# Performance work log

Measured on AMD Instinct MI355X. Metric: run time of the kernel, lower is better.

The kernel has to match this reference:

```python
import jax, jax.numpy as jnp
import numpy as np

B, T, D, K = 16, 2048, 256, 1024


def setup_inputs() -> dict:
    key = jax.random.key(0)
    k1, k2 = jax.random.split(key)
    z_e_x = jax.random.normal(k1, (B, T, D), dtype=jnp.float32)
    # torch init is uniform(-1/K, 1/K); use normal scaled similarly for a realistic trained codebook
    embedding = jax.random.normal(k2, (K, D), dtype=jnp.float32)
    return {"z_e_x": z_e_x, "embedding": embedding}


def _vq_indices(inputs_flat, codebook):
    codebook_sqr = jnp.sum(codebook * codebook, axis=1)            # [K]
    inputs_sqr = jnp.sum(inputs_flat * inputs_flat, axis=1, keepdims=True)  # [N,1]
    distances = inputs_sqr + codebook_sqr[None, :] - 2.0 * (inputs_flat @ codebook.T)  # [N,K]
    return jnp.argmin(distances, axis=1)                           # [N] int


def reference(z_e_x, embedding):
    Dd = embedding.shape[1]
    inputs_flat = z_e_x.reshape(-1, Dd)                 # [N, D]
    indices_flat = _vq_indices(inputs_flat, embedding)  # [N]
    codes = embedding[indices_flat].reshape(z_e_x.shape)  # gather lookup
    z_q_x = codes                                       # straight-through quantized output
    z_q_x_bar = codes                                   # eval mode: embedding unchanged, same gather
    indices = indices_flat.reshape(z_e_x.shape[:-1])
    return (z_q_x, z_q_x_bar, indices)
```

## Files before the change

### kernel.cpp

```cpp
#include <hip/hip_runtime.h>
#include <float.h>

constexpr int kD = 256;
constexpr int kK = 1024;
constexpr int kN = 16 * 2048;

using bf16x8 = __attribute__((ext_vector_type(8))) short;
using f32x16 = __attribute__((ext_vector_type(16))) float;
using u16x8  = __attribute__((ext_vector_type(8))) unsigned short;

__device__ __forceinline__ unsigned short f2bf(float x) {
    union { float f; unsigned u; } a; a.f = x;
    const unsigned u = a.u;
    return (unsigned short)((u + 0x7fffu + ((u >> 16) & 1u)) >> 16);
}
__device__ __forceinline__ float bf2f(unsigned short b) {
    union { unsigned u; float f; } a; a.u = ((unsigned)b) << 16;
    return a.f;
}

#define GLOAD_LDS16(GP, LP) \
    __builtin_amdgcn_global_load_lds((const __attribute__((address_space(1))) unsigned int*)(GP), \
                                     (__attribute__((address_space(3))) unsigned int*)(LP), 16, 0, 0)

__global__ void vq_split_kernel(const float* __restrict__ src,
                                unsigned short* __restrict__ oh,
                                unsigned short* __restrict__ om,
                                unsigned short* __restrict__ ol) {
    const int RB = blockIdx.x;
    const int t  = threadIdx.x;
    #pragma unroll
    for (int it = 0; it < 8; ++it) {
        const int u   = it * 256 + t;
        const int l   = u & 63;
        const int f   = (u >> 6) & 1;
        const int t16 = u >> 7;
        const int row = RB * 64 + f * 32 + (l & 31);
        const int d0  = t16 * 16 + (l >> 5) * 8;
        const float4 v0 = *reinterpret_cast<const float4*>(src + (size_t)row * kD + d0);
        const float4 v1 = *reinterpret_cast<const float4*>(src + (size_t)row * kD + d0 + 4);
        const float x[8] = {v0.x, v0.y, v0.z, v0.w, v1.x, v1.y, v1.z, v1.w};
        u16x8 H, M, L;
        #pragma unroll
        for (int e = 0; e < 8; ++e) {
            const unsigned short h = f2bf(x[e]);
            const float r1 = x[e] - bf2f(h);
            const unsigned short m = f2bf(r1);
            const float r2 = r1 - bf2f(m);
            const unsigned short lo = f2bf(r2);
            H[e] = (short)h; M[e] = (short)m; L[e] = (short)lo;
        }
        const size_t o = (size_t)RB * 16384 + (size_t)u * 8;
        *reinterpret_cast<u16x8*>(oh + o) = H;
        *reinterpret_cast<u16x8*>(om + o) = M;
        *reinterpret_cast<u16x8*>(ol + o) = L;
    }
}

__global__ void vq_csqr_kernel(const float* __restrict__ E, float* __restrict__ csqr) {
    const int k = blockIdx.x * 4 + (threadIdx.x >> 6);
    const int lane = threadIdx.x & 63;
    const float4 v = reinterpret_cast<const float4*>(E + (size_t)k * kD)[lane];
    float s = v.x * v.x + v.y * v.y + v.z * v.z + v.w * v.w;
    #pragma unroll
    for (int off = 32; off > 0; off >>= 1) s += __shfl_down(s, off);
    if (lane == 0) csqr[k] = s;
}

__global__ __launch_bounds__(256, 3) void vq_gemm_kernel(
    const unsigned short* __restrict__ xh, const unsigned short* __restrict__ xm,
    const unsigned short* __restrict__ xl,
    const unsigned short* __restrict__ eh, const unsigned short* __restrict__ em,
    const unsigned short* __restrict__ el,
    const float* __restrict__ csqr,
    float* __restrict__ cand_val, int* __restrict__ cand_idx)
{
    __shared__ bf16x8 smem[3072];
    const int tid  = threadIdx.x;
    const int lane = tid & 63;
    const int wid  = tid >> 6;
    const int wr   = wid >> 1;
    const int wc   = wid & 1;

    const int w    = blockIdx.x;
    const int xcd  = w & 7;
    const int slot = w >> 3;
    const int rb   = xcd * 32 + (slot >> 3);
    const int cb   = slot & 7;

    f32x16 acc00 = {}, acc01 = {}, acc10 = {}, acc11 = {};

    for (int c = 0; c < 8; ++c) {
        __syncthreads();
        #pragma unroll
        for (int k2 = 0; k2 < 12; ++k2) {
            const int sg  = wid + k2 * 4;
            const bool isB = sg >= 24;
            const int q  = isB ? sg - 24 : sg;
            const int f  = q & 1, tt = (q >> 1) & 1, g = (q >> 2) & 1, s = q >> 3;
            const unsigned short* base = isB ? (s == 0 ? eh : s == 1 ? em : el)
                                             : (s == 0 ? xh : s == 1 ? xm : xl);
            const int RBx = (isB ? cb : rb) * 2 + g;
            const size_t unit = ((size_t)(RBx * 16 + c * 2 + tt) * 2 + f) * 512 + lane * 8;
            GLOAD_LDS16(base + unit, &smem[sg * 64]);
        }
        __syncthreads();

        #pragma unroll
        for (int tt = 0; tt < 2; ++tt) {
            const int ab = wr * 256 + tt * 128 + lane;
            const int bb = 1536 + wc * 256 + tt * 128 + lane;
            const bf16x8 ah0 = smem[ab];            const bf16x8 ah1 = smem[ab + 64];
            const bf16x8 am0 = smem[ab + 512];      const bf16x8 am1 = smem[ab + 576];
            const bf16x8 al0 = smem[ab + 1024];     const bf16x8 al1 = smem[ab + 1088];
            const bf16x8 bh0 = smem[bb];            const bf16x8 bh1 = smem[bb + 64];
            const bf16x8 bm0 = smem[bb + 512];      const bf16x8 bm1 = smem[bb + 576];
            const bf16x8 bl0 = smem[bb + 1024];     const bf16x8 bl1 = smem[bb + 1088];
#define MFMA(A,B,C) __builtin_amdgcn_mfma_f32_32x32x16_bf16(A, B, C, 0, 0, 0)
            acc00 = MFMA(ah0, bh0, acc00); acc01 = MFMA(ah0, bh1, acc01);
            acc10 = MFMA(ah1, bh0, acc10); acc11 = MFMA(ah1, bh1, acc11);
            acc00 = MFMA(ah0, bm0, acc00); acc01 = MFMA(ah0, bm1, acc01);
            acc10 = MFMA(ah1, bm0, acc10); acc11 = MFMA(ah1, bm1, acc11);
            acc00 = MFMA(am0, bh0, acc00); acc01 = MFMA(am0, bh1, acc01);
            acc10 = MFMA(am1, bh0, acc10); acc11 = MFMA(am1, bh1, acc11);
            acc00 = MFMA(ah0, bl0, acc00); acc01 = MFMA(ah0, bl1, acc01);
            acc10 = MFMA(ah1, bl0, acc10); acc11 = MFMA(ah1, bl1, acc11);
            acc00 = MFMA(al0, bh0, acc00); acc01 = MFMA(al0, bh1, acc01);
            acc10 = MFMA(al1, bh0, acc10); acc11 = MFMA(al1, bh1, acc11);
            acc00 = MFMA(am0, bm0, acc00); acc01 = MFMA(am0, bm1, acc01);
            acc10 = MFMA(am1, bm0, acc10); acc11 = MFMA(am1, bm1, acc11);
#undef MFMA
        }
    }

    const int colA  = cb * 128 + wc * 64 + (lane & 31);
    const float csA = csqr[colA];
    const float csB = csqr[colA + 32];
    const int rbase = rb * 128 + wr * 64 + 4 * (lane >> 5);
    const int cslot = cb * 2 + wc;

    #pragma unroll
    for (int half = 0; half < 2; ++half) {
        #pragma unroll
        for (int r = 0; r < 16; ++r) {
            const float s0 = (half == 0) ? acc00[r] : acc10[r];
            const float s1 = (half == 0) ? acc01[r] : acc11[r];
            float bv = fmaf(-2.0f, s0, csA);
            int   bi = colA;
            const float v1 = fmaf(-2.0f, s1, csB);
            if (v1 < bv) { bv = v1; bi = colA + 32; }
            #pragma unroll
            for (int mk = 16; mk >= 1; mk >>= 1) {
                const float ov = __shfl_xor(bv, mk);
                const int   oi = __shfl_xor(bi, mk);
                if (ov < bv || (ov == bv && oi < bi)) { bv = ov; bi = oi; }
            }
            if ((lane & 31) == 0) {
                const int row = rbase + half * 32 + (r & 3) + 8 * (r >> 2);
                cand_val[(size_t)cslot * kN + row] = bv;
                cand_idx[(size_t)cslot * kN + row] = bi;
            }
        }
    }
}

__global__ void vq_combine_kernel(const float* __restrict__ cand_val,
                                  const int* __restrict__ cand_idx,
                                  int* __restrict__ idx, float* __restrict__ idxf)
{
    const int row = blockIdx.x * 256 + threadIdx.x;
    float bv = cand_val[row];
    int   bi = cand_idx[row];
    #pragma unroll
    for (int s = 1; s < 16; ++s) {
        const float v = cand_val[(size_t)s * kN + row];
        const int  i2 = cand_idx[(size_t)s * kN + row];
        if (v < bv || (v == bv && i2 < bi)) { bv = v; bi = i2; }
    }
    idx[row]  = bi;
    idxf[row] = (float)bi;
}

__global__ void vq_gather_kernel(const float* __restrict__ E, const int* __restrict__ idx,
                                 float* __restrict__ zq, float* __restrict__ zqb) {
    const int row = blockIdx.x * 4 + (threadIdx.x >> 6);
    const int lane = threadIdx.x & 63;
    const int k = idx[row];
    const float4 v = reinterpret_cast<const float4*>(E + (size_t)k * kD)[lane];
    reinterpret_cast<float4*>(zq + (size_t)row * kD)[lane] = v;
    reinterpret_cast<float4*>(zqb + (size_t)row * kD)[lane] = v;
}

extern "C" void kernel_launch(void* const* d_in, const int* in_sizes, int n_in,
                              void* d_out, int out_size, void* d_ws, size_t ws_size,
                              hipStream_t stream) {
    const float* X = (const float*)d_in[0];
    const float* E = (const float*)d_in[1];

    float* out  = (float*)d_out;
    float* zq   = out;
    float* zqb  = out + (size_t)kN * kD;
    float* idxf = out + 2 * (size_t)kN * kD;

    char* ob = (char*)d_out;
    unsigned short* XIh = (unsigned short*)ob;
    unsigned short* XIm = XIh + (size_t)kN * kD;
    unsigned short* XIl = XIm + (size_t)kN * kD;
    float* cand_val = (float*)(ob + 3ull * kN * kD * 2);
    int*   cand_idx = (int*)(ob + 3ull * kN * kD * 2 + 16ull * kN * 4);

    char* ws = (char*)d_ws;
    float* csqr = (float*)ws;
    unsigned short* EIh = (unsigned short*)(ws + 4096);
    unsigned short* EIm = EIh + (size_t)kK * kD;
    unsigned short* EIl = EIm + (size_t)kK * kD;
    int* idx = (int*)(ws + 4096 + 3ull * kK * kD * 2);

    vq_split_kernel<<<kN / 64, 256, 0, stream>>>(X, XIh, XIm, XIl);
    vq_split_kernel<<<kK / 64, 256, 0, stream>>>(E, EIh, EIm, EIl);
    vq_csqr_kernel<<<kK / 4, 256, 0, stream>>>(E, csqr);
    vq_gemm_kernel<<<(kN / 128) * (kK / 128), 256, 0, stream>>>(
        XIh, XIm, XIl, EIh, EIm, EIl, csqr, cand_val, cand_idx);
    vq_combine_kernel<<<kN / 256, 256, 0, stream>>>(cand_val, cand_idx, idx, idxf);
    vq_gather_kernel<<<kN / 4, 256, 0, stream>>>(E, idx, zq, zqb);
}
```

Before: 243.6 us.

## Enlarge GEMM tile to 256x128, double-buffer LDS, fuse codebook split with norms

The distance GEMM moves from 128x128 tiles to 256x128 tiles, giving each wave 4x2 accumulators so A and B fragments are reused across more MFMAs. The K loop now runs 16 steps of 16 and double-buffers LDS, issuing the next chunk's global-to-LDS loads before computing on the current one, which drops one barrier per iteration. The codebook split and the codebook squared-norm kernels are fused into a single launch. The costs are more registers (launch bounds lowered to 2 blocks per CU), a larger LDS footprint, and half as many GEMM blocks.

```diff
diff --git a/kernel.cpp b/kernel.cpp
--- a/kernel.cpp
+++ b/kernel.cpp
@@ -57,17 +57,54 @@
     }
 }
 
-__global__ void vq_csqr_kernel(const float* __restrict__ E, float* __restrict__ csqr) {
-    const int k = blockIdx.x * 4 + (threadIdx.x >> 6);
-    const int lane = threadIdx.x & 63;
-    const float4 v = reinterpret_cast<const float4*>(E + (size_t)k * kD)[lane];
-    float s = v.x * v.x + v.y * v.y + v.z * v.z + v.w * v.w;
-    #pragma unroll
-    for (int off = 32; off > 0; off >>= 1) s += __shfl_down(s, off);
-    if (lane == 0) csqr[k] = s;
-}
-
-__global__ __launch_bounds__(256, 3) void vq_gemm_kernel(
+__global__ void vq_split_csqr_kernel(const float* __restrict__ src,
+                                     unsigned short* __restrict__ oh,
+                                     unsigned short* __restrict__ om,
+                                     unsigned short* __restrict__ ol,
+                                     float* __restrict__ csqr) {
+    __shared__ float part[64][4];
+    const int RB = blockIdx.x;
+    const int t  = threadIdx.x;
+    #pragma unroll
+    for (int it = 0; it < 8; ++it) {
+        const int u   = it * 256 + t;
+        const int l   = u & 63;
+        const int f   = (u >> 6) & 1;
+        const int t16 = u >> 7;
+        const int row = RB * 64 + f * 32 + (l & 31);
+        const int d0  = t16 * 16 + (l >> 5) * 8;
+        const float4 v0 = *reinterpret_cast<const float4*>(src + (size_t)row * kD + d0);
+        const float4 v1 = *reinterpret_cast<const float4*>(src + (size_t)row * kD + d0 + 4);
+        const float x[8] = {v0.x, v0.y, v0.z, v0.w, v1.x, v1.y, v1.z, v1.w};
+        u16x8 H, M, L;
+        #pragma unroll
+        for (int e = 0; e < 8; ++e) {
+            const unsigned short h = f2bf(x[e]);
+            const float r1 = x[e] - bf2f(h);
+            const unsigned short m = f2bf(r1);
+            const float r2 = r1 - bf2f(m);
+            const unsigned short lo = f2bf(r2);
+            H[e] = (short)h; M[e] = (short)m; L[e] = (short)lo;
+        }
+        const size_t o = (size_t)RB * 16384 + (size_t)u * 8;
+        *reinterpret_cast<u16x8*>(oh + o) = H;
+        *reinterpret_cast<u16x8*>(om + o) = M;
+        *reinterpret_cast<u16x8*>(ol + o) = L;
+    }
+    const int r = t >> 2, q = t & 3;
+    const float* rp = src + (size_t)(RB * 64 + r) * kD + q * 64;
+    float s = 0.0f;
+    #pragma unroll
+    for (int i = 0; i < 16; ++i) {
+        const float4 v = reinterpret_cast<const float4*>(rp)[i];
+        s += v.x * v.x + v.y * v.y + v.z * v.z + v.w * v.w;
+    }
+    part[r][q] = s;
+    __syncthreads();
+    if (t < 64) csqr[RB * 64 + t] = part[t][0] + part[t][1] + part[t][2] + part[t][3];
+}
+
+__global__ __launch_bounds__(256, 2) void vq_gemm_kernel(
     const unsigned short* __restrict__ xh, const unsigned short* __restrict__ xm,
     const unsigned short* __restrict__ xl,
     const unsigned short* __restrict__ eh, const unsigned short* __restrict__ em,
@@ -75,7 +112,7 @@
     const float* __restrict__ csqr,
     float* __restrict__ cand_val, int* __restrict__ cand_idx)
 {
-    __shared__ bf16x8 smem[3072];
+    __shared__ bf16x8 smem[2][2304];
     const int tid  = threadIdx.x;
     const int lane = tid & 63;
     const int wid  = tid >> 6;
@@ -85,70 +122,88 @@
     const int w    = blockIdx.x;
     const int xcd  = w & 7;
     const int slot = w >> 3;
-    const int rb   = xcd * 32 + (slot >> 3);
-    const int cb   = slot & 7;
-
-    f32x16 acc00 = {}, acc01 = {}, acc10 = {}, acc11 = {};
-
-    for (int c = 0; c < 8; ++c) {
+    const int rbp  = xcd * 16 + (slot >> 3);
+    const int cbp  = slot & 7;
+
+    const unsigned short* gbase[9];
+    int ldsoff[9];
+    #pragma unroll
+    for (int k2 = 0; k2 < 9; ++k2) {
+        const int s = wid * 9 + k2;
+        const bool isB = s >= 24;
+        const int q   = isB ? s - 24 : s;
+        const int grp = q / 6;
+        const int rem = q % 6;
+        const int f   = rem / 3;
+        const int lv  = rem % 3;
+        const unsigned short* img = isB ? (lv == 0 ? eh : lv == 1 ? em : el)
+                                        : (lv == 0 ? xh : lv == 1 ? xm : xl);
+        const int RBx = isB ? (cbp * 2 + grp) : (rbp * 4 + grp);
+        gbase[k2] = img + (size_t)RBx * 16384 + f * 512 + lane * 8;
+        ldsoff[k2] = (isB ? 1536 + q * 64 : q * 64);
+    }
+
+    f32x16 acc[4][2];
+    #pragma unroll
+    for (int m = 0; m < 4; ++m) { acc[m][0] = (f32x16)0.0f; acc[m][1] = (f32x16)0.0f; }
+
+    int au[4], bu[2];
+    #pragma unroll
+    for (int m = 0; m < 4; ++m) au[m] = ((wr * 2 + (m >> 1)) * 6 + (m & 1) * 3) * 64 + lane;
+    #pragma unroll
+    for (int n = 0; n < 2; ++n) bu[n] = 1536 + (wc * 6 + n * 3) * 64 + lane;
+
+    #pragma unroll
+    for (int k2 = 0; k2 < 9; ++k2) GLOAD_LDS16(gbase[k2], &smem[0][ldsoff[k2]]);
+    __syncthreads();
+
+    for (int c = 0; c < 16; ++c) {
+        const int cur = c & 1;
+        if (c < 15) {
+            #pragma unroll
+            for (int k2 = 0; k2 < 9; ++k2)
+                GLOAD_LDS16(gbase[k2] + (size_t)(c + 1) * 1024, &smem[cur ^ 1][ldsoff[k2]]);
+        }
+        const bf16x8* sb = smem[cur];
+        bf16x8 A[3][4];
+        #pragma unroll
+        for (int m = 0; m < 4; ++m) {
+            A[0][m] = sb[au[m]]; A[1][m] = sb[au[m] + 64]; A[2][m] = sb[au[m] + 128];
+        }
+#define MFMA(a, b, cacc) __builtin_amdgcn_mfma_f32_32x32x16_bf16(a, b, cacc, 0, 0, 0)
+        #pragma unroll
+        for (int n = 0; n < 2; ++n) {
+            const bf16x8 bh = sb[bu[n]], bm = sb[bu[n] + 64], bl = sb[bu[n] + 128];
+            #pragma unroll
+            for (int m = 0; m < 4; ++m) {
+                f32x16 a5 = acc[m][n];
+                a5 = MFMA(A[0][m], bh, a5);
+                a5 = MFMA(A[0][m], bm, a5);
+                a5 = MFMA(A[1][m], bh, a5);
+                a5 = MFMA(A[0][m], bl, a5);
+                a5 = MFMA(A[2][m], bh, a5);
+                a5 = MFMA(A[1][m], bm, a5);
+                acc[m][n] = a5;
+            }
+        }
+#undef MFMA
         __syncthreads();
-        #pragma unroll
-        for (int k2 = 0; k2 < 12; ++k2) {
-            const int sg  = wid + k2 * 4;
-            const bool isB = sg >= 24;
-            const int q  = isB ? sg - 24 : sg;
-            const int f  = q & 1, tt = (q >> 1) & 1, g = (q >> 2) & 1, s = q >> 3;
-            const unsigned short* base = isB ? (s == 0 ? eh : s == 1 ? em : el)
-                                             : (s == 0 ? xh : s == 1 ? xm : xl);
-            const int RBx = (isB ? cb : rb) * 2 + g;
-            const size_t unit = ((size_t)(RBx * 16 + c * 2 + tt) * 2 + f) * 512 + lane * 8;
-            GLOAD_LDS16(base + unit, &smem[sg * 64]);
-        }
-        __syncthreads();
-
-        #pragma unroll
-        for (int tt = 0; tt < 2; ++tt) {
-            const int ab = wr * 256 + tt * 128 + lane;
-            const int bb = 1536 + wc * 256 + tt * 128 + lane;
-            const bf16x8 ah0 = smem[ab];            const bf16x8 ah1 = smem[ab + 64];
-            const bf16x8 am0 = smem[ab + 512];      const bf16x8 am1 = smem[ab + 576];
-            const bf16x8 al0 = smem[ab + 1024];     const bf16x8 al1 = smem[ab + 1088];
-            const bf16x8 bh0 = smem[bb];            const bf16x8 bh1 = smem[bb + 64];
-            const bf16x8 bm0 = smem[bb + 512];      const bf16x8 bm1 = smem[bb + 576];
-            const bf16x8 bl0 = smem[bb + 1024];     const bf16x8 bl1 = smem[bb + 1088];
-#define MFMA(A,B,C) __builtin_amdgcn_mfma_f32_32x32x16_bf16(A, B, C, 0, 0, 0)
-            acc00 = MFMA(ah0, bh0, acc00); acc01 = MFMA(ah0, bh1, acc01);
-            acc10 = MFMA(ah1, bh0, acc10); acc11 = MFMA(ah1, bh1, acc11);
-            acc00 = MFMA(ah0, bm0, acc00); acc01 = MFMA(ah0, bm1, acc01);
-            acc10 = MFMA(ah1, bm0, acc10); acc11 = MFMA(ah1, bm1, acc11);
-            acc00 = MFMA(am0, bh0, acc00); acc01 = MFMA(am0, bh1, acc01);
-            acc10 = MFMA(am1, bh0, acc10); acc11 = MFMA(am1, bh1, acc11);
-            acc00 = MFMA(ah0, bl0, acc00); acc01 = MFMA(ah0, bl1, acc01);
-            acc10 = MFMA(ah1, bl0, acc10); acc11 = MFMA(ah1, bl1, acc11);
-            acc00 = MFMA(al0, bh0, acc00); acc01 = MFMA(al0, bh1, acc01);
-            acc10 = MFMA(al1, bh0, acc10); acc11 = MFMA(al1, bh1, acc11);
-            acc00 = MFMA(am0, bm0, acc00); acc01 = MFMA(am0, bm1, acc01);
-            acc10 = MFMA(am1, bm0, acc10); acc11 = MFMA(am1, bm1, acc11);
-#undef MFMA
-        }
-    }
-
-    const int colA  = cb * 128 + wc * 64 + (lane & 31);
-    const float csA = csqr[colA];
-    const float csB = csqr[colA + 32];
-    const int rbase = rb * 128 + wr * 64 + 4 * (lane >> 5);
-    const int cslot = cb * 2 + wc;
-
-    #pragma unroll
-    for (int half = 0; half < 2; ++half) {
+    }
+
+    const int colbase = cbp * 128 + wc * 64;
+    const float cs0 = csqr[colbase + (lane & 31)];
+    const float cs1 = csqr[colbase + 32 + (lane & 31)];
+    const int rowbase = rbp * 256 + wr * 128 + 4 * (lane >> 5);
+    const int cslot = cbp * 2 + wc;
+
+    #pragma unroll
+    for (int m = 0; m < 4; ++m) {
         #pragma unroll
         for (int r = 0; r < 16; ++r) {
-            const float s0 = (half == 0) ? acc00[r] : acc10[r];
-            const float s1 = (half == 0) ? acc01[r] : acc11[r];
-            float bv = fmaf(-2.0f, s0, csA);
-            int   bi = colA;
-            const float v1 = fmaf(-2.0f, s1, csB);
-            if (v1 < bv) { bv = v1; bi = colA + 32; }
+            float bv = fmaf(-2.0f, acc[m][0][r], cs0);
+            int   bi = colbase + (lane & 31);
+            const float v1 = fmaf(-2.0f, acc[m][1][r], cs1);
+            if (v1 < bv) { bv = v1; bi = colbase + 32 + (lane & 31); }
             #pragma unroll
             for (int mk = 16; mk >= 1; mk >>= 1) {
                 const float ov = __shfl_xor(bv, mk);
@@ -156,7 +211,7 @@
                 if (ov < bv || (ov == bv && oi < bi)) { bv = ov; bi = oi; }
             }
             if ((lane & 31) == 0) {
-                const int row = rbase + half * 32 + (r & 3) + 8 * (r >> 2);
+                const int row = rowbase + m * 32 + (r & 3) + 8 * (r >> 2);
                 cand_val[(size_t)cslot * kN + row] = bv;
                 cand_idx[(size_t)cslot * kN + row] = bi;
             }
@@ -217,9 +272,8 @@
     int* idx = (int*)(ws + 4096 + 3ull * kK * kD * 2);
 
     vq_split_kernel<<<kN / 64, 256, 0, stream>>>(X, XIh, XIm, XIl);
-    vq_split_kernel<<<kK / 64, 256, 0, stream>>>(E, EIh, EIm, EIl);
-    vq_csqr_kernel<<<kK / 4, 256, 0, stream>>>(E, csqr);
-    vq_gemm_kernel<<<(kN / 128) * (kK / 128), 256, 0, stream>>>(
+    vq_split_csqr_kernel<<<kK / 64, 256, 0, stream>>>(E, EIh, EIm, EIl, csqr);
+    vq_gemm_kernel<<<(kN / 256) * (kK / 128), 256, 0, stream>>>(
         XIh, XIm, XIl, EIh, EIm, EIl, csqr, cand_val, cand_idx);
     vq_combine_kernel<<<kN / 256, 256, 0, stream>>>(cand_val, cand_idx, idx, idxf);
     vq_gather_kernel<<<kN / 4, 256, 0, stream>>>(E, idx, zq, zqb);
```

Result: slower. 255.5 us (+4.9%).
